# Performance work log

Measured on AMD Instinct MI355X. Metric: run time of the kernel, lower is better.

Reference implementation:

```python
import jax, jax.numpy as jnp
import numpy as np

RES, GATE, SKIP, K, DIL, CIN = 128, 256, 128, 3, 2, 80
PAD = (K - 1) * DIL


def _wn(v, g):
    # weight_norm: w = g * v / ||v||, norm over all dims except dim 0 (out_channels)
    norm = jnp.sqrt(jnp.sum(v * v, axis=(1, 2), keepdims=True))
    return v * (g.reshape(-1, 1, 1) / norm)


def setup_inputs() -> dict:
    key = jax.random.key(0)
    ks = jax.random.split(key, 12)
    s = lambda *sh: 1.0 / np.sqrt(np.prod(sh[1:]))
    d = {
        "x": jax.random.normal(ks[0], (8, RES, 32768), dtype=jnp.float32),
        "condition": jax.random.normal(ks[1], (8, CIN, 32768), dtype=jnp.float32),
        "conv_v": jax.random.normal(ks[2], (GATE, RES, K), dtype=jnp.float32) * s(GATE, RES, K),
        "conv_g": jnp.ones((GATE,), dtype=jnp.float32),
        "conv_b": jnp.zeros((GATE,), dtype=jnp.float32),
        "lc_v": jax.random.normal(ks[3], (GATE, CIN, 1), dtype=jnp.float32) * s(GATE, CIN, 1),
        "lc_g": jnp.ones((GATE,), dtype=jnp.float32),
        "skip_v": jax.random.normal(ks[4], (SKIP, GATE // 2, 1), dtype=jnp.float32) * s(SKIP, GATE // 2, 1),
        "skip_g": jnp.ones((SKIP,), dtype=jnp.float32),
        "skip_b": jnp.zeros((SKIP,), dtype=jnp.float32),
        "out_v": jax.random.normal(ks[5], (RES, GATE // 2, 1), dtype=jnp.float32) * s(RES, GATE // 2, 1),
        "out_g": jnp.ones((RES,), dtype=jnp.float32),
        "out_b": jnp.zeros((RES,), dtype=jnp.float32),
    }
    return d


def reference(x, condition, conv_v, conv_g, conv_b, lc_v, lc_g,
              skip_v, skip_g, skip_b, out_v, out_g, out_b):
    residual = x
    w = _wn(conv_v, conv_g)  # [GATE, RES, K]
    # torch pads symmetrically then slices [:, :, :-PAD]; equivalent to left-only pad
    h = jax.lax.conv_general_dilated(
        x, w, window_strides=(1,), padding=[(PAD, 0)], rhs_dilation=(DIL,),
        dimension_numbers=("NCH", "OIH", "NCH"))
    h = h + conv_b[None, :, None]  # [B, GATE, T]
    a, b = jnp.split(h, 2, axis=1)
    lc_w = _wn(lc_v, lc_g)[:, :, 0]  # [GATE, CIN]
    c = jnp.einsum("oc,bct->bot", lc_w, condition)
    ca, cb = jnp.split(c, 2, axis=1)
    g = jnp.tanh(a + ca) * jax.nn.sigmoid(b + cb)  # [B, GATE//2, T]
    skip_w = _wn(skip_v, skip_g)[:, :, 0]
    s = jnp.einsum("oc,bct->bot", skip_w, g) + skip_b[None, :, None]
    out_w = _wn(out_v, out_g)[:, :, 0]
    o = jnp.einsum("oc,bct->bot", out_w, g) + out_b[None, :, None]
    return (o + residual, s)
```

## Files before the change

### kernel.cpp

```cpp
#include <hip/hip_runtime.h>

#define B_N   8
#define T_N   32768
#define RESC  128
#define GATEC 256
#define CINC  80
#define CINP  96
#define NT    64
#define HALO  4
#define XROWS 68

#define XSTR_B 272
#define CSTR_B 208
#define CS_OFF 18496
#define LDS_BYTES (18496 + 13312)

#define AP1_ELEMS (16*12*512)
#define AP2_ELEMS (16*3*512)
#define AP3_ELEMS (16*4*512)

#define OFF_S ((size_t)B_N * RESC * T_N)

typedef __attribute__((ext_vector_type(8))) short short8;
typedef __attribute__((ext_vector_type(4))) float f32x4;

__device__ __forceinline__ ushort f2bf(float f) {
  union { float f; unsigned int u; } c; c.f = f;
  unsigned int u = c.u;
  u += 0x7fffu + ((u >> 16) & 1u);
  return (ushort)(u >> 16);
}

__device__ __forceinline__ char* lds_at(char* base, int row, int strB, int colB) {
  int off = row * strB + colB;
  off ^= ((row >> 3) & 7) << 4;
  return base + off;
}

__global__ __launch_bounds__(256) void wn_pack_kernel(
    const float* __restrict__ conv_v, const float* __restrict__ conv_g,
    const float* __restrict__ lc_v,  const float* __restrict__ lc_g,
    const float* __restrict__ skip_v,const float* __restrict__ skip_g,
    const float* __restrict__ out_v, const float* __restrict__ out_g,
    ushort* __restrict__ Ap1, ushort* __restrict__ Ap2, ushort* __restrict__ Ap3) {
  const int o   = blockIdx.x;
  const int tid = threadIdx.x;
  const int mtg = o >> 4, r = o & 15;
  __shared__ float red[256];

  float s = 0.f;
  for (int e = tid; e < RESC * 3; e += 256) { float v = conv_v[o * RESC * 3 + e]; s += v * v; }
  red[tid] = s; __syncthreads();
  for (int off = 128; off > 0; off >>= 1) { if (tid < off) red[tid] += red[tid + off]; __syncthreads(); }
  const float csc = conv_g[o] / sqrtf(red[0]);
  __syncthreads();
  for (int e = tid; e < 384; e += 256) {
    const int ks = e >> 5, q = (e >> 3) & 3, j = e & 7;
    const int tap = ks >> 2, ci = (ks & 3) * 32 + q * 8 + j;
    Ap1[((mtg * 12 + ks) * 64 + q * 16 + r) * 8 + j] = f2bf(conv_v[(o * RESC + ci) * 3 + tap] * csc);
  }

  s = 0.f;
  for (int e = tid; e < CINC; e += 256) { float v = lc_v[o * CINC + e]; s += v * v; }
  red[tid] = s; __syncthreads();
  for (int off = 128; off > 0; off >>= 1) { if (tid < off) red[tid] += red[tid + off]; __syncthreads(); }
  const float lsc = lc_g[o] / sqrtf(red[0]);
  __syncthreads();
  for (int e = tid; e < CINP; e += 256) {
    const int ks = e >> 5, q = (e >> 3) & 3, j = e & 7;
    const float wv = (e < CINC) ? lc_v[o * CINC + e] * lsc : 0.f;
    Ap2[((mtg * 3 + ks) * 64 + q * 16 + r) * 8 + j] = f2bf(wv);
  }

  const float* vrow = (o < 128) ? (skip_v + o * 128) : (out_v + (o - 128) * 128);
  const float  gg   = (o < 128) ? skip_g[o] : out_g[o - 128];
  s = 0.f;
  for (int e = tid; e < 128; e += 256) { float v = vrow[e]; s += v * v; }
  red[tid] = s; __syncthreads();
  for (int off = 128; off > 0; off >>= 1) { if (tid < off) red[tid] += red[tid + off]; __syncthreads(); }
  const float ssc = gg / sqrtf(red[0]);
  for (int e = tid; e < 128; e += 256) {
    const int ks = e >> 5, q = (e >> 3) & 3, j = e & 7;
    Ap3[((mtg * 4 + ks) * 64 + q * 16 + r) * 8 + j] = f2bf(vrow[e] * ssc);
  }
}

__global__ __launch_bounds__(512) void fused_block_kernel(
    const float* __restrict__ x, const float* __restrict__ cond,
    const float* __restrict__ conv_b, const float* __restrict__ skip_b,
    const float* __restrict__ out_b,
    const ushort* __restrict__ Ap1, const ushort* __restrict__ Ap2,
    const ushort* __restrict__ Ap3,
    float* __restrict__ out) {
  const int tid  = threadIdx.x;
  const int w    = tid >> 6;
  const int lane = tid & 63;
  const int q    = lane >> 4;
  const int n    = lane & 15;
  const int blk  = blockIdx.x;
  const int b    = blk >> 9;
  const int t0   = (blk & 511) << 6;

  __shared__ __align__(128) char smem[LDS_BYTES];
  char* xs = smem;
  char* cs = smem + CS_OFF;
  char* gs = smem;

  if (tid < 256) {
    const int c0 = (tid >> 3) << 2;
    const int tt = (tid & 7) << 3;
    const float* xp = x + ((size_t)b * RESC + c0) * T_N + t0 + tt;
    float va[4][8];
#pragma unroll
    for (int rr = 0; rr < 4; ++rr) {
      const float4* rp = (const float4*)(xp + (size_t)rr * T_N);
      const float4 a0 = rp[0], a1 = rp[1];
      va[rr][0] = a0.x; va[rr][1] = a0.y; va[rr][2] = a0.z; va[rr][3] = a0.w;
      va[rr][4] = a1.x; va[rr][5] = a1.y; va[rr][6] = a1.z; va[rr][7] = a1.w;
    }
#pragma unroll
    for (int ss = 0; ss < 8; ++ss) {
      const unsigned lo = (unsigned)f2bf(va[0][ss]) | ((unsigned)f2bf(va[1][ss]) << 16);
      const unsigned hi = (unsigned)f2bf(va[2][ss]) | ((unsigned)f2bf(va[3][ss]) << 16);
      *(uint2*)lds_at(xs, HALO + tt + ss, XSTR_B, c0 * 2) = make_uint2(lo, hi);
    }
  } else if (tid < 448) {
    const int e  = tid - 256;
    const int c0 = (e >> 3) << 2;
    const int tt = (e & 7) << 3;
    if (c0 < CINC) {
      const float* cp = cond + ((size_t)b * CINC + c0) * T_N + t0 + tt;
      float va[4][8];
#pragma unroll
      for (int rr = 0; rr < 4; ++rr) {
        const float4* rp = (const float4*)(cp + (size_t)rr * T_N);
        const float4 a0 = rp[0], a1 = rp[1];
        va[rr][0] = a0.x; va[rr][1] = a0.y; va[rr][2] = a0.z; va[rr][3] = a0.w;
        va[rr][4] = a1.x; va[rr][5] = a1.y; va[rr][6] = a1.z; va[rr][7] = a1.w;
      }
#pragma unroll
      for (int ss = 0; ss < 8; ++ss) {
        const unsigned lo = (unsigned)f2bf(va[0][ss]) | ((unsigned)f2bf(va[1][ss]) << 16);
        const unsigned hi = (unsigned)f2bf(va[2][ss]) | ((unsigned)f2bf(va[3][ss]) << 16);
        *(uint2*)lds_at(cs, tt + ss, CSTR_B, c0 * 2) = make_uint2(lo, hi);
      }
    } else {
#pragma unroll
      for (int ss = 0; ss < 8; ++ss)
        *(uint2*)lds_at(cs, tt + ss, CSTR_B, c0 * 2) = make_uint2(0u, 0u);
    }
  } else {
    const int e   = tid - 448;
    const int ch0 = e << 1;
    float h0[4] = {0.f, 0.f, 0.f, 0.f}, h1[4] = {0.f, 0.f, 0.f, 0.f};
    if (t0 > 0) {
      const float4 v0 = *(const float4*)(x + ((size_t)b * RESC + ch0) * T_N + t0 - 4);
      const float4 v1 = *(const float4*)(x + ((size_t)b * RESC + ch0 + 1) * T_N + t0 - 4);
      h0[0] = v0.x; h0[1] = v0.y; h0[2] = v0.z; h0[3] = v0.w;
      h1[0] = v1.x; h1[1] = v1.y; h1[2] = v1.z; h1[3] = v1.w;
    }
#pragma unroll
    for (int rr = 0; rr < 4; ++rr) {
      const unsigned pk = (unsigned)f2bf(h0[rr]) | ((unsigned)f2bf(h1[rr]) << 16);
      *(unsigned int*)lds_at(xs, rr, XSTR_B, ch0 * 2) = pk;
    }
  }
  __syncthreads();

  const int mtA = w, mtB = 8 + w;
  f32x4 acc[2][4];
  {
    const float4 ca = *(const float4*)(conv_b + mtA * 16 + q * 4);
    const float4 cb = *(const float4*)(conv_b + mtB * 16 + q * 4);
#pragma unroll
    for (int nt = 0; nt < 4; ++nt) {
      acc[0][nt] = (f32x4){ca.x, ca.y, ca.z, ca.w};
      acc[1][nt] = (f32x4){cb.x, cb.y, cb.z, cb.w};
    }
  }
#pragma unroll
  for (int ks = 0; ks < 12; ++ks) {
    const int tap = ks >> 2;
    const int cbyte = ((ks & 3) << 6);
    const short8 af0 = *(const short8*)(Ap1 + ((mtA * 12 + ks) * 64 + lane) * 8);
    const short8 af1 = *(const short8*)(Ap1 + ((mtB * 12 + ks) * 64 + lane) * 8);
    short8 bfr[4];
#pragma unroll
    for (int nt = 0; nt < 4; ++nt)
      bfr[nt] = *(const short8*)lds_at(xs, nt * 16 + n + tap * 2, XSTR_B, cbyte + q * 16);
#pragma unroll
    for (int nt = 0; nt < 4; ++nt) {
      acc[0][nt] = __builtin_amdgcn_mfma_f32_16x16x32_bf16(af0, bfr[nt], acc[0][nt], 0, 0, 0);
      acc[1][nt] = __builtin_amdgcn_mfma_f32_16x16x32_bf16(af1, bfr[nt], acc[1][nt], 0, 0, 0);
    }
  }
#pragma unroll
  for (int ks = 0; ks < 3; ++ks) {
    const short8 af0 = *(const short8*)(Ap2 + ((mtA * 3 + ks) * 64 + lane) * 8);
    const short8 af1 = *(const short8*)(Ap2 + ((mtB * 3 + ks) * 64 + lane) * 8);
    short8 bfr[4];
#pragma unroll
    for (int nt = 0; nt < 4; ++nt)
      bfr[nt] = *(const short8*)lds_at(cs, nt * 16 + n, CSTR_B, ks * 64 + q * 16);
#pragma unroll
    for (int nt = 0; nt < 4; ++nt) {
      acc[0][nt] = __builtin_amdgcn_mfma_f32_16x16x32_bf16(af0, bfr[nt], acc[0][nt], 0, 0, 0);
      acc[1][nt] = __builtin_amdgcn_mfma_f32_16x16x32_bf16(af1, bfr[nt], acc[1][nt], 0, 0, 0);
    }
  }
  __syncthreads();

#pragma unroll
  for (int nt = 0; nt < 4; ++nt) {
    const f32x4 va = acc[0][nt];
    const f32x4 vb = acc[1][nt];
    float r[4];
#pragma unroll
    for (int i = 0; i < 4; ++i) {
      const float ta = 1.f - 2.f / (__expf(2.f * va[i]) + 1.f);
      const float sb = 1.f / (1.f + __expf(-vb[i]));
      r[i] = ta * sb;
    }
    const unsigned lo = (unsigned)f2bf(r[0]) | ((unsigned)f2bf(r[1]) << 16);
    const unsigned hi = (unsigned)f2bf(r[2]) | ((unsigned)f2bf(r[3]) << 16);
    *(uint2*)lds_at(gs, nt * 16 + n, XSTR_B, (16 * w + 4 * q) * 2) = make_uint2(lo, hi);
  }
  __syncthreads();

  {
    const float4 bs = *(const float4*)(skip_b + w * 16 + q * 4);
    const float4 bo = *(const float4*)(out_b  + w * 16 + q * 4);
#pragma unroll
    for (int nt = 0; nt < 4; ++nt) {
      acc[0][nt] = (f32x4){bs.x, bs.y, bs.z, bs.w};
      acc[1][nt] = (f32x4){bo.x, bo.y, bo.z, bo.w};
    }
  }
#pragma unroll
  for (int ks = 0; ks < 4; ++ks) {
    const short8 af0 = *(const short8*)(Ap3 + ((w * 4 + ks) * 64 + lane) * 8);
    const short8 af1 = *(const short8*)(Ap3 + (((8 + w) * 4 + ks) * 64 + lane) * 8);
    short8 bfr[4];
#pragma unroll
    for (int nt = 0; nt < 4; ++nt)
      bfr[nt] = *(const short8*)lds_at(gs, nt * 16 + n, XSTR_B, ks * 64 + q * 16);
#pragma unroll
    for (int nt = 0; nt < 4; ++nt) {
      acc[0][nt] = __builtin_amdgcn_mfma_f32_16x16x32_bf16(af0, bfr[nt], acc[0][nt], 0, 0, 0);
      acc[1][nt] = __builtin_amdgcn_mfma_f32_16x16x32_bf16(af1, bfr[nt], acc[1][nt], 0, 0, 0);
    }
  }

  const int ch = 16 * w + 4 * q;
#pragma unroll
  for (int nt = 0; nt < 4; ++nt) {
    const int t = t0 + nt * 16 + n;
    const f32x4 vs = acc[0][nt];
    const f32x4 vo = acc[1][nt];
    float* ds = out + OFF_S + ((size_t)(b * RESC + ch)) * T_N + t;
#pragma unroll
    for (int i = 0; i < 4; ++i) ds[(size_t)i * T_N] = vs[i];
    const float* xr = x + ((size_t)(b * RESC + ch)) * T_N + t;
    float* dо = out + ((size_t)(b * RESC + ch)) * T_N + t;
#pragma unroll
    for (int i = 0; i < 4; ++i) dо[(size_t)i * T_N] = vo[i] + xr[(size_t)i * T_N];
  }
}

extern "C" void kernel_launch(void* const* d_in, const int* in_sizes, int n_in,
                              void* d_out, int out_size, void* d_ws, size_t ws_size,
                              hipStream_t stream) {
  const float* x      = (const float*)d_in[0];
  const float* cond   = (const float*)d_in[1];
  const float* conv_v = (const float*)d_in[2];
  const float* conv_g = (const float*)d_in[3];
  const float* conv_b = (const float*)d_in[4];
  const float* lc_v   = (const float*)d_in[5];
  const float* lc_g   = (const float*)d_in[6];
  const float* skip_v = (const float*)d_in[7];
  const float* skip_g = (const float*)d_in[8];
  const float* skip_b = (const float*)d_in[9];
  const float* out_v  = (const float*)d_in[10];
  const float* out_g  = (const float*)d_in[11];
  const float* out_b  = (const float*)d_in[12];

  ushort* Ap1 = (ushort*)d_ws;
  ushort* Ap2 = Ap1 + AP1_ELEMS;
  ushort* Ap3 = Ap2 + AP2_ELEMS;

  hipLaunchKernelGGL(wn_pack_kernel, dim3(256), dim3(256), 0, stream,
                     conv_v, conv_g, lc_v, lc_g, skip_v, skip_g, out_v, out_g,
                     Ap1, Ap2, Ap3);
  hipLaunchKernelGGL(fused_block_kernel, dim3(4096), dim3(512), 0, stream,
                     x, cond, conv_b, skip_b, out_b, Ap1, Ap2, Ap3, (float*)d_out);
}
```

Before: 504.2 us.

## Process four time tiles per block with register-prefetched next tile

Each block now loops over four consecutive 64-step time tiles, and the grid shrinks from 4096 to 1024 blocks. While the current tile's MFMAs run, the next tile's x, condition and halo loads are issued into registers and written to LDS after the epilogue, overlapping global latency with compute. Gate math also switches from division to hardware reciprocal. The cost is more registers and extra barriers per tile, and fewer blocks to hide latency across CUs.

```diff
diff --git a/kernel.cpp b/kernel.cpp
--- a/kernel.cpp
+++ b/kernel.cpp
@@ -9,6 +9,7 @@
 #define NT    64
 #define HALO  4
 #define XROWS 68
+#define TPB   4
 
 #define XSTR_B 272
 #define CSTR_B 208
@@ -29,6 +30,10 @@
   unsigned int u = c.u;
   u += 0x7fffu + ((u >> 16) & 1u);
   return (ushort)(u >> 16);
+}
+
+__device__ __forceinline__ float f4e(const float4 v, int i) {
+  return i == 0 ? v.x : i == 1 ? v.y : i == 2 ? v.z : v.w;
 }
 
 __device__ __forceinline__ char* lds_at(char* base, int row, int strB, int colB) {
@@ -98,172 +103,248 @@
   const int q    = lane >> 4;
   const int n    = lane & 15;
   const int blk  = blockIdx.x;
-  const int b    = blk >> 9;
-  const int t0   = (blk & 511) << 6;
+  const int b    = blk >> 7;
+  const int t0base = (blk & 127) << 8;
 
   __shared__ __align__(128) char smem[LDS_BYTES];
   char* xs = smem;
   char* cs = smem + CS_OFF;
   char* gs = smem;
 
-  if (tid < 256) {
-    const int c0 = (tid >> 3) << 2;
-    const int tt = (tid & 7) << 3;
-    const float* xp = x + ((size_t)b * RESC + c0) * T_N + t0 + tt;
-    float va[4][8];
-#pragma unroll
-    for (int rr = 0; rr < 4; ++rr) {
-      const float4* rp = (const float4*)(xp + (size_t)rr * T_N);
-      const float4 a0 = rp[0], a1 = rp[1];
-      va[rr][0] = a0.x; va[rr][1] = a0.y; va[rr][2] = a0.z; va[rr][3] = a0.w;
-      va[rr][4] = a1.x; va[rr][5] = a1.y; va[rr][6] = a1.z; va[rr][7] = a1.w;
-    }
-#pragma unroll
-    for (int ss = 0; ss < 8; ++ss) {
-      const unsigned lo = (unsigned)f2bf(va[0][ss]) | ((unsigned)f2bf(va[1][ss]) << 16);
-      const unsigned hi = (unsigned)f2bf(va[2][ss]) | ((unsigned)f2bf(va[3][ss]) << 16);
-      *(uint2*)lds_at(xs, HALO + tt + ss, XSTR_B, c0 * 2) = make_uint2(lo, hi);
-    }
-  } else if (tid < 448) {
-    const int e  = tid - 256;
-    const int c0 = (e >> 3) << 2;
-    const int tt = (e & 7) << 3;
-    if (c0 < CINC) {
-      const float* cp = cond + ((size_t)b * CINC + c0) * T_N + t0 + tt;
-      float va[4][8];
+  const int sc0 = (tid < 256) ? ((tid >> 3) << 2) : (((tid - 256) >> 3) << 2);
+  const int stt = (tid < 256) ? ((tid & 7) << 3) : (((tid - 256) & 7) << 3);
+
+  {
+    const int t0 = t0base;
+    if (tid < 256) {
+      const float* xp = x + ((size_t)b * RESC + sc0) * T_N + t0 + stt;
+      float4 va[8];
 #pragma unroll
       for (int rr = 0; rr < 4; ++rr) {
-        const float4* rp = (const float4*)(cp + (size_t)rr * T_N);
-        const float4 a0 = rp[0], a1 = rp[1];
-        va[rr][0] = a0.x; va[rr][1] = a0.y; va[rr][2] = a0.z; va[rr][3] = a0.w;
-        va[rr][4] = a1.x; va[rr][5] = a1.y; va[rr][6] = a1.z; va[rr][7] = a1.w;
+        const float4* rp = (const float4*)(xp + (size_t)rr * T_N);
+        va[rr * 2 + 0] = rp[0]; va[rr * 2 + 1] = rp[1];
       }
 #pragma unroll
       for (int ss = 0; ss < 8; ++ss) {
-        const unsigned lo = (unsigned)f2bf(va[0][ss]) | ((unsigned)f2bf(va[1][ss]) << 16);
-        const unsigned hi = (unsigned)f2bf(va[2][ss]) | ((unsigned)f2bf(va[3][ss]) << 16);
-        *(uint2*)lds_at(cs, tt + ss, CSTR_B, c0 * 2) = make_uint2(lo, hi);
+        const int h4 = ss >> 2, l4 = ss & 3;
+        const unsigned lo = (unsigned)f2bf(f4e(va[0 + h4], l4)) | ((unsigned)f2bf(f4e(va[2 + h4], l4)) << 16);
+        const unsigned hi = (unsigned)f2bf(f4e(va[4 + h4], l4)) | ((unsigned)f2bf(f4e(va[6 + h4], l4)) << 16);
+        *(uint2*)lds_at(xs, HALO + stt + ss, XSTR_B, sc0 * 2) = make_uint2(lo, hi);
+      }
+    } else if (tid < 448) {
+      if (sc0 < CINC) {
+        const float* cp = cond + ((size_t)b * CINC + sc0) * T_N + t0 + stt;
+        float4 va[8];
+#pragma unroll
+        for (int rr = 0; rr < 4; ++rr) {
+          const float4* rp = (const float4*)(cp + (size_t)rr * T_N);
+          va[rr * 2 + 0] = rp[0]; va[rr * 2 + 1] = rp[1];
+        }
+#pragma unroll
+        for (int ss = 0; ss < 8; ++ss) {
+          const int h4 = ss >> 2, l4 = ss & 3;
+          const unsigned lo = (unsigned)f2bf(f4e(va[0 + h4], l4)) | ((unsigned)f2bf(f4e(va[2 + h4], l4)) << 16);
+          const unsigned hi = (unsigned)f2bf(f4e(va[4 + h4], l4)) | ((unsigned)f2bf(f4e(va[6 + h4], l4)) << 16);
+          *(uint2*)lds_at(cs, stt + ss, CSTR_B, sc0 * 2) = make_uint2(lo, hi);
+        }
+      } else {
+#pragma unroll
+        for (int ss = 0; ss < 8; ++ss)
+          *(uint2*)lds_at(cs, stt + ss, CSTR_B, sc0 * 2) = make_uint2(0u, 0u);
       }
     } else {
-#pragma unroll
-      for (int ss = 0; ss < 8; ++ss)
-        *(uint2*)lds_at(cs, tt + ss, CSTR_B, c0 * 2) = make_uint2(0u, 0u);
-    }
-  } else {
-    const int e   = tid - 448;
-    const int ch0 = e << 1;
-    float h0[4] = {0.f, 0.f, 0.f, 0.f}, h1[4] = {0.f, 0.f, 0.f, 0.f};
-    if (t0 > 0) {
-      const float4 v0 = *(const float4*)(x + ((size_t)b * RESC + ch0) * T_N + t0 - 4);
-      const float4 v1 = *(const float4*)(x + ((size_t)b * RESC + ch0 + 1) * T_N + t0 - 4);
-      h0[0] = v0.x; h0[1] = v0.y; h0[2] = v0.z; h0[3] = v0.w;
-      h1[0] = v1.x; h1[1] = v1.y; h1[2] = v1.z; h1[3] = v1.w;
-    }
-#pragma unroll
-    for (int rr = 0; rr < 4; ++rr) {
-      const unsigned pk = (unsigned)f2bf(h0[rr]) | ((unsigned)f2bf(h1[rr]) << 16);
-      *(unsigned int*)lds_at(xs, rr, XSTR_B, ch0 * 2) = pk;
+      const int ch0 = (tid - 448) << 1;
+      float4 v0 = make_float4(0.f, 0.f, 0.f, 0.f), v1 = v0;
+      if (t0 > 0) {
+        v0 = *(const float4*)(x + ((size_t)b * RESC + ch0) * T_N + t0 - 4);
+        v1 = *(const float4*)(x + ((size_t)b * RESC + ch0 + 1) * T_N + t0 - 4);
+      }
+#pragma unroll
+      for (int rr = 0; rr < 4; ++rr) {
+        const unsigned pkh = (unsigned)f2bf(f4e(v0, rr)) | ((unsigned)f2bf(f4e(v1, rr)) << 16);
+        *(unsigned int*)lds_at(xs, rr, XSTR_B, ch0 * 2) = pkh;
+      }
     }
   }
   __syncthreads();
 
   const int mtA = w, mtB = 8 + w;
-  f32x4 acc[2][4];
-  {
-    const float4 ca = *(const float4*)(conv_b + mtA * 16 + q * 4);
-    const float4 cb = *(const float4*)(conv_b + mtB * 16 + q * 4);
+  int t0 = t0base;
+  float4 pend[8];
+  unsigned pk[16];
+
+#pragma unroll 1
+  for (int it = 0; it < TPB; ++it) {
+    const bool more = (it + 1 < TPB);
+
+    f32x4 acc[2][4];
+    {
+      const float4 ca = *(const float4*)(conv_b + mtA * 16 + q * 4);
+      const float4 cb = *(const float4*)(conv_b + mtB * 16 + q * 4);
+#pragma unroll
+      for (int nt = 0; nt < 4; ++nt) {
+        acc[0][nt] = (f32x4){ca.x, ca.y, ca.z, ca.w};
+        acc[1][nt] = (f32x4){cb.x, cb.y, cb.z, cb.w};
+      }
+    }
+#pragma unroll
+    for (int ks = 0; ks < 12; ++ks) {
+      const int tap = ks >> 2;
+      const int cbyte = ((ks & 3) << 6);
+      const short8 af0 = *(const short8*)(Ap1 + ((mtA * 12 + ks) * 64 + lane) * 8);
+      const short8 af1 = *(const short8*)(Ap1 + ((mtB * 12 + ks) * 64 + lane) * 8);
+      short8 bfr[4];
+#pragma unroll
+      for (int nt = 0; nt < 4; ++nt)
+        bfr[nt] = *(const short8*)lds_at(xs, nt * 16 + n + tap * 2, XSTR_B, cbyte + q * 16);
+#pragma unroll
+      for (int nt = 0; nt < 4; ++nt) {
+        acc[0][nt] = __builtin_amdgcn_mfma_f32_16x16x32_bf16(af0, bfr[nt], acc[0][nt], 0, 0, 0);
+        acc[1][nt] = __builtin_amdgcn_mfma_f32_16x16x32_bf16(af1, bfr[nt], acc[1][nt], 0, 0, 0);
+      }
+    }
+
+    if (more) {
+      const int t1 = t0 + NT;
+      if (tid < 256) {
+        const float* xp = x + ((size_t)b * RESC + sc0) * T_N + t1 + stt;
+#pragma unroll
+        for (int rr = 0; rr < 4; ++rr) {
+          const float4* rp = (const float4*)(xp + (size_t)rr * T_N);
+          pend[rr * 2 + 0] = rp[0]; pend[rr * 2 + 1] = rp[1];
+        }
+      } else if (tid < 448) {
+        if (sc0 < CINC) {
+          const float* cp = cond + ((size_t)b * CINC + sc0) * T_N + t1 + stt;
+#pragma unroll
+          for (int rr = 0; rr < 4; ++rr) {
+            const float4* rp = (const float4*)(cp + (size_t)rr * T_N);
+            pend[rr * 2 + 0] = rp[0]; pend[rr * 2 + 1] = rp[1];
+          }
+        }
+      } else {
+        const int ch0 = (tid - 448) << 1;
+        pend[0] = *(const float4*)(x + ((size_t)b * RESC + ch0) * T_N + t1 - 4);
+        pend[1] = *(const float4*)(x + ((size_t)b * RESC + ch0 + 1) * T_N + t1 - 4);
+      }
+    }
+
+#pragma unroll
+    for (int ks = 0; ks < 3; ++ks) {
+      const short8 af0 = *(const short8*)(Ap2 + ((mtA * 3 + ks) * 64 + lane) * 8);
+      const short8 af1 = *(const short8*)(Ap2 + ((mtB * 3 + ks) * 64 + lane) * 8);
+      short8 bfr[4];
+#pragma unroll
+      for (int nt = 0; nt < 4; ++nt)
+        bfr[nt] = *(const short8*)lds_at(cs, nt * 16 + n, CSTR_B, ks * 64 + q * 16);
+#pragma unroll
+      for (int nt = 0; nt < 4; ++nt) {
+        acc[0][nt] = __builtin_amdgcn_mfma_f32_16x16x32_bf16(af0, bfr[nt], acc[0][nt], 0, 0, 0);
+        acc[1][nt] = __builtin_amdgcn_mfma_f32_16x16x32_bf16(af1, bfr[nt], acc[1][nt], 0, 0, 0);
+      }
+    }
+    __syncthreads();
+
 #pragma unroll
     for (int nt = 0; nt < 4; ++nt) {
-      acc[0][nt] = (f32x4){ca.x, ca.y, ca.z, ca.w};
-      acc[1][nt] = (f32x4){cb.x, cb.y, cb.z, cb.w};
-    }
-  }
-#pragma unroll
-  for (int ks = 0; ks < 12; ++ks) {
-    const int tap = ks >> 2;
-    const int cbyte = ((ks & 3) << 6);
-    const short8 af0 = *(const short8*)(Ap1 + ((mtA * 12 + ks) * 64 + lane) * 8);
-    const short8 af1 = *(const short8*)(Ap1 + ((mtB * 12 + ks) * 64 + lane) * 8);
-    short8 bfr[4];
-#pragma unroll
-    for (int nt = 0; nt < 4; ++nt)
-      bfr[nt] = *(const short8*)lds_at(xs, nt * 16 + n + tap * 2, XSTR_B, cbyte + q * 16);
-#pragma unroll
-    for (int nt = 0; nt < 4; ++nt) {
-      acc[0][nt] = __builtin_amdgcn_mfma_f32_16x16x32_bf16(af0, bfr[nt], acc[0][nt], 0, 0, 0);
-      acc[1][nt] = __builtin_amdgcn_mfma_f32_16x16x32_bf16(af1, bfr[nt], acc[1][nt], 0, 0, 0);
-    }
-  }
-#pragma unroll
-  for (int ks = 0; ks < 3; ++ks) {
-    const short8 af0 = *(const short8*)(Ap2 + ((mtA * 3 + ks) * 64 + lane) * 8);
-    const short8 af1 = *(const short8*)(Ap2 + ((mtB * 3 + ks) * 64 + lane) * 8);
-    short8 bfr[4];
-#pragma unroll
-    for (int nt = 0; nt < 4; ++nt)
-      bfr[nt] = *(const short8*)lds_at(cs, nt * 16 + n, CSTR_B, ks * 64 + q * 16);
-#pragma unroll
-    for (int nt = 0; nt < 4; ++nt) {
-      acc[0][nt] = __builtin_amdgcn_mfma_f32_16x16x32_bf16(af0, bfr[nt], acc[0][nt], 0, 0, 0);
-      acc[1][nt] = __builtin_amdgcn_mfma_f32_16x16x32_bf16(af1, bfr[nt], acc[1][nt], 0, 0, 0);
-    }
-  }
-  __syncthreads();
-
-#pragma unroll
-  for (int nt = 0; nt < 4; ++nt) {
-    const f32x4 va = acc[0][nt];
-    const f32x4 vb = acc[1][nt];
-    float r[4];
-#pragma unroll
-    for (int i = 0; i < 4; ++i) {
-      const float ta = 1.f - 2.f / (__expf(2.f * va[i]) + 1.f);
-      const float sb = 1.f / (1.f + __expf(-vb[i]));
-      r[i] = ta * sb;
-    }
-    const unsigned lo = (unsigned)f2bf(r[0]) | ((unsigned)f2bf(r[1]) << 16);
-    const unsigned hi = (unsigned)f2bf(r[2]) | ((unsigned)f2bf(r[3]) << 16);
-    *(uint2*)lds_at(gs, nt * 16 + n, XSTR_B, (16 * w + 4 * q) * 2) = make_uint2(lo, hi);
-  }
-  __syncthreads();
-
-  {
-    const float4 bs = *(const float4*)(skip_b + w * 16 + q * 4);
-    const float4 bo = *(const float4*)(out_b  + w * 16 + q * 4);
-#pragma unroll
-    for (int nt = 0; nt < 4; ++nt) {
-      acc[0][nt] = (f32x4){bs.x, bs.y, bs.z, bs.w};
-      acc[1][nt] = (f32x4){bo.x, bo.y, bo.z, bo.w};
-    }
-  }
-#pragma unroll
-  for (int ks = 0; ks < 4; ++ks) {
-    const short8 af0 = *(const short8*)(Ap3 + ((w * 4 + ks) * 64 + lane) * 8);
-    const short8 af1 = *(const short8*)(Ap3 + (((8 + w) * 4 + ks) * 64 + lane) * 8);
-    short8 bfr[4];
-#pragma unroll
-    for (int nt = 0; nt < 4; ++nt)
-      bfr[nt] = *(const short8*)lds_at(gs, nt * 16 + n, XSTR_B, ks * 64 + q * 16);
-#pragma unroll
-    for (int nt = 0; nt < 4; ++nt) {
-      acc[0][nt] = __builtin_amdgcn_mfma_f32_16x16x32_bf16(af0, bfr[nt], acc[0][nt], 0, 0, 0);
-      acc[1][nt] = __builtin_amdgcn_mfma_f32_16x16x32_bf16(af1, bfr[nt], acc[1][nt], 0, 0, 0);
-    }
-  }
-
-  const int ch = 16 * w + 4 * q;
-#pragma unroll
-  for (int nt = 0; nt < 4; ++nt) {
-    const int t = t0 + nt * 16 + n;
-    const f32x4 vs = acc[0][nt];
-    const f32x4 vo = acc[1][nt];
-    float* ds = out + OFF_S + ((size_t)(b * RESC + ch)) * T_N + t;
-#pragma unroll
-    for (int i = 0; i < 4; ++i) ds[(size_t)i * T_N] = vs[i];
-    const float* xr = x + ((size_t)(b * RESC + ch)) * T_N + t;
-    float* dо = out + ((size_t)(b * RESC + ch)) * T_N + t;
-#pragma unroll
-    for (int i = 0; i < 4; ++i) dо[(size_t)i * T_N] = vo[i] + xr[(size_t)i * T_N];
+      const f32x4 va = acc[0][nt];
+      const f32x4 vb = acc[1][nt];
+      float r[4];
+#pragma unroll
+      for (int i = 0; i < 4; ++i) {
+        const float ta = 1.f - 2.f * __builtin_amdgcn_rcpf(__expf(2.f * va[i]) + 1.f);
+        const float sb = __builtin_amdgcn_rcpf(1.f + __expf(-vb[i]));
+        r[i] = ta * sb;
+      }
+      const unsigned lo = (unsigned)f2bf(r[0]) | ((unsigned)f2bf(r[1]) << 16);
+      const unsigned hi = (unsigned)f2bf(r[2]) | ((unsigned)f2bf(r[3]) << 16);
+      *(uint2*)lds_at(gs, nt * 16 + n, XSTR_B, (16 * w + 4 * q) * 2) = make_uint2(lo, hi);
+    }
+
+    if (more) {
+      if (tid < 448) {
+        if (tid < 256 || sc0 < CINC) {
+#pragma unroll
+          for (int ss = 0; ss < 8; ++ss) {
+            const int h4 = ss >> 2, l4 = ss & 3;
+            pk[ss * 2 + 0] = (unsigned)f2bf(f4e(pend[0 + h4], l4)) |
+                             ((unsigned)f2bf(f4e(pend[2 + h4], l4)) << 16);
+            pk[ss * 2 + 1] = (unsigned)f2bf(f4e(pend[4 + h4], l4)) |
+                             ((unsigned)f2bf(f4e(pend[6 + h4], l4)) << 16);
+          }
+        }
+      } else {
+#pragma unroll
+        for (int rr = 0; rr < 4; ++rr)
+          pk[rr] = (unsigned)f2bf(f4e(pend[0], rr)) | ((unsigned)f2bf(f4e(pend[1], rr)) << 16);
+      }
+    }
+    __syncthreads();
+
+    {
+      const float4 bs = *(const float4*)(skip_b + w * 16 + q * 4);
+      const float4 bo = *(const float4*)(out_b  + w * 16 + q * 4);
+#pragma unroll
+      for (int nt = 0; nt < 4; ++nt) {
+        acc[0][nt] = (f32x4){bs.x, bs.y, bs.z, bs.w};
+        acc[1][nt] = (f32x4){bo.x, bo.y, bo.z, bo.w};
+      }
+    }
+#pragma unroll
+    for (int ks = 0; ks < 4; ++ks) {
+      const short8 af0 = *(const short8*)(Ap3 + ((w * 4 + ks) * 64 + lane) * 8);
+      const short8 af1 = *(const short8*)(Ap3 + (((8 + w) * 4 + ks) * 64 + lane) * 8);
+      short8 bfr[4];
+#pragma unroll
+      for (int nt = 0; nt < 4; ++nt)
+        bfr[nt] = *(const short8*)lds_at(gs, nt * 16 + n, XSTR_B, ks * 64 + q * 16);
+#pragma unroll
+      for (int nt = 0; nt < 4; ++nt) {
+        acc[0][nt] = __builtin_amdgcn_mfma_f32_16x16x32_bf16(af0, bfr[nt], acc[0][nt], 0, 0, 0);
+        acc[1][nt] = __builtin_amdgcn_mfma_f32_16x16x32_bf16(af1, bfr[nt], acc[1][nt], 0, 0, 0);
+      }
+    }
+
+    {
+      const int ch = 16 * w + 4 * q;
+#pragma unroll
+      for (int nt = 0; nt < 4; ++nt) {
+        const int t = t0 + nt * 16 + n;
+        const f32x4 vs = acc[0][nt];
+        const f32x4 vo = acc[1][nt];
+        float* ds = out + OFF_S + ((size_t)(b * RESC + ch)) * T_N + t;
+#pragma unroll
+        for (int i = 0; i < 4; ++i) ds[(size_t)i * T_N] = vs[i];
+        const float* xr = x + ((size_t)(b * RESC + ch)) * T_N + t;
+        float* dp = out + ((size_t)(b * RESC + ch)) * T_N + t;
+#pragma unroll
+        for (int i = 0; i < 4; ++i) dp[(size_t)i * T_N] = vo[i] + xr[(size_t)i * T_N];
+      }
+    }
+
+    if (more) {
+      __syncthreads();
+      if (tid < 256) {
+#pragma unroll
+        for (int ss = 0; ss < 8; ++ss)
+          *(uint2*)lds_at(xs, HALO + stt + ss, XSTR_B, sc0 * 2) =
+              make_uint2(pk[ss * 2], pk[ss * 2 + 1]);
+      } else if (tid < 448) {
+        if (sc0 < CINC) {
+#pragma unroll
+          for (int ss = 0; ss < 8; ++ss)
+            *(uint2*)lds_at(cs, stt + ss, CSTR_B, sc0 * 2) =
+                make_uint2(pk[ss * 2], pk[ss * 2 + 1]);
+        }
+      } else {
+        const int ch0 = (tid - 448) << 1;
+#pragma unroll
+        for (int rr = 0; rr < 4; ++rr)
+          *(unsigned int*)lds_at(xs, rr, XSTR_B, ch0 * 2) = pk[rr];
+      }
+      __syncthreads();
+    }
+    t0 += NT;
   }
 }
 
@@ -291,6 +372,6 @@
   hipLaunchKernelGGL(wn_pack_kernel, dim3(256), dim3(256), 0, stream,
                      conv_v, conv_g, lc_v, lc_g, skip_v, skip_g, out_v, out_g,
                      Ap1, Ap2, Ap3);
-  hipLaunchKernelGGL(fused_block_kernel, dim3(4096), dim3(512), 0, stream,
+  hipLaunchKernelGGL(fused_block_kernel, dim3(1024), dim3(512), 0, stream,
                      x, cond, conv_b, skip_b, out_b, Ap1, Ap2, Ap3, (float*)d_out);
 }
```

Result: slower. 896.4 us (+77.8%).
